# Optimization experiments

Hardware: AMD Instinct MI355X
Metric: run time of the kernel (lower is better)

Reference implementation:

```python
import jax, jax.numpy as jnp
import numpy as np

B, C, T = 128, 8, 128   # batch, channels, time steps
K, S = 20, 128          # known classes, barycenter length


def setup_inputs() -> dict:
    key = jax.random.key(0)
    k1, k2, k3, k4, k5 = jax.random.split(key, 5)
    x = jax.random.normal(k1, (B, C, T), dtype=jnp.float32)
    preds = jax.random.randint(k2, (B,), 0, K).astype(jnp.int32)
    barycenters = jax.random.normal(k3, (K, S, C), dtype=jnp.float32)
    # thresholds centered near realistic scales so both detector branches fire
    top_dist = 7.0 + 0.5 * jax.random.normal(k4, (K,), dtype=jnp.float32)
    bottom_cc = 25.0 + 5.0 * jax.random.normal(k5, (K, C), dtype=jnp.float32)
    return {"x": x, "preds": preds, "barycenters": barycenters,
            "top_dist": top_dist, "bottom_cc": bottom_cc}


def _dtw_dist(cost):
    """Classic DTW DP over a [T, S] sq-euclidean cost matrix; returns accumulated cost."""
    inf = jnp.asarray(jnp.inf, cost.dtype)
    row0 = jnp.cumsum(cost[0])  # first row: only left moves

    def row_step(prev, crow):
        prev_shift = jnp.concatenate([jnp.full((1,), inf, cost.dtype), prev[:-1]])
        def col_step(left, inp):
            c, p, ps = inp
            v = c + jnp.minimum(jnp.minimum(p, ps), left)
            return v, v
        _, row = jax.lax.scan(col_step, inf, (crow, prev, prev_shift))
        return row, None

    last, _ = jax.lax.scan(row_step, row0, cost[1:])
    return last[-1]


def reference(x, preds, barycenters, top_dist, bottom_cc):
    xt = jnp.transpose(x, (0, 2, 1))                    # [B, T, C]
    x2 = jnp.sum(xt * xt, axis=-1)                      # [B, T]
    b2 = jnp.sum(barycenters * barycenters, axis=-1)    # [K, S]
    dots = jnp.einsum('btc,ksc->bkts', xt, barycenters)  # [B, K, T, S]
    cost = jnp.maximum(x2[:, None, :, None] + b2[None, :, None, :] - 2.0 * dots, 0.0)

    Bn, Kn, Tn, Sn = cost.shape
    dists = jax.vmap(_dtw_dist)(cost.reshape(Bn * Kn, Tn, Sn)).reshape(Bn, Kn)
    log_dists = jnp.log(dists)
    dtw_unknown = jnp.all(log_dists > top_dist[None, :], axis=1)   # [B]

    # per-channel full cross-correlation max vs each barycenter
    corr_max = lambda a, v: jnp.max(jnp.correlate(a, v, mode='full'))
    per_ch = jax.vmap(corr_max, in_axes=(1, 1))          # over channels -> [C]
    per_cls = jax.vmap(per_ch, in_axes=(None, 0))        # over classes  -> [K, C]
    per_b = jax.vmap(per_cls, in_axes=(0, None))         # over batch    -> [B, K, C]
    ccs = per_b(xt, barycenters)
    # class 'fails' if any channel cc is not above its bottom threshold
    cc_unknown = jnp.all(jnp.any(ccs <= bottom_cc[None, :, :], axis=2), axis=1)  # [B]

    unknown = cc_unknown | dtw_unknown
    return jnp.where(unknown, Kn, preds)
```

## Files before the change

kernel.cpp:

```cpp
#include <hip/hip_runtime.h>
#include <hip/hip_bf16.h>
#include <math.h>

#define B_ 128
#define C_ 8
#define T_ 128
#define K_ 20
#define S_ 128

#define XROW 388
#define BTROW 132
#define SWZ(j) ((j) ^ ((((j) >> 5) & 7) << 2))
#define XP_GUARD 16
#define BT_BASE (4 * XROW + XP_GUARD)
#define TILEF 1536
#define SMEMF 3680

template <int CTRL, int RMASK>
__device__ __forceinline__ float dppf(float oldv, float v) {
    return __int_as_float(__builtin_amdgcn_update_dpp(
        __float_as_int(oldv), __float_as_int(v), CTRL, RMASK, 0xf, false));
}

__global__ __launch_bounds__(256) void fused_kernel(const float* __restrict__ x,
                                                    const float* __restrict__ bary,
                                                    const float* __restrict__ top_dist,
                                                    const float* __restrict__ bottom_cc,
                                                    int* __restrict__ dtw_gt,
                                                    int* __restrict__ cc_fail2) {
    __shared__ __align__(16) float smem[SMEMF];
    const float INF = __builtin_inff();
    int u = blockIdx.x;
    int tid = threadIdx.x;
    int w = tid >> 6;
    int lane = tid & 63;

    if (u % 5 == 0) {
        int j  = u / 5;
        int p0 = j * 8 + w * 2;
        int b  = p0 / K_;
        int k0 = p0 - b * K_;
        int b_lo = (j * 8) / K_;
        int b_hi = (j * 8 + 7) / K_;
        float* tile0 = smem;
        float* tile1 = smem + TILEF;

        {
            int c  = tid >> 5;
            int t0 = (tid & 31) * 4;
            float4 v0 = *(const float4*)(x + ((size_t)b_lo * C_ + c) * T_ + t0);
            float4 v1 = *(const float4*)(x + ((size_t)b_hi * C_ + c) * T_ + t0);
            tile0[(t0 + 0) * 12 + c] = v0.x;
            tile0[(t0 + 1) * 12 + c] = v0.y;
            tile0[(t0 + 2) * 12 + c] = v0.z;
            tile0[(t0 + 3) * 12 + c] = v0.w;
            tile1[(t0 + 0) * 12 + c] = v1.x;
            tile1[(t0 + 1) * 12 + c] = v1.y;
            tile1[(t0 + 2) * 12 + c] = v1.z;
            tile1[(t0 + 3) * 12 + c] = v1.w;
        }
        __syncthreads();
        {
            float* tt = (tid < T_) ? tile0 : tile1;
            int t = tid & (T_ - 1);
            const float* rp = tt + t * 12;
            float4 xa = *(const float4*)rp;
            float4 xh = *(const float4*)(rp + 4);
            float s = xa.x * xa.x;
            s = fmaf(xa.y, xa.y, s); s = fmaf(xa.z, xa.z, s); s = fmaf(xa.w, xa.w, s);
            s = fmaf(xh.x, xh.x, s); s = fmaf(xh.y, xh.y, s); s = fmaf(xh.z, xh.z, s);
            s = fmaf(xh.w, xh.w, s);
            tt[t * 12 + 8] = s;
        }
        __syncthreads();

        const float* tile = (b == b_lo) ? tile0 : tile1;

        float bvA0[8], bvA1[8], bvB0[8], bvB1[8], B2A0, B2A1, B2B0, B2B1;
        {
            const float4* bpA = (const float4*)(bary + ((size_t)k0 * S_ + 2 * lane) * C_);
            const float4* bpB = (const float4*)(bary + ((size_t)(k0 + 1) * S_ + 2 * lane) * C_);
            float4 qa0 = bpA[0], qa1 = bpA[1], qa2 = bpA[2], qa3 = bpA[3];
            float4 qb0 = bpB[0], qb1 = bpB[1], qb2 = bpB[2], qb3 = bpB[3];
            bvA0[0]=qa0.x; bvA0[1]=qa0.y; bvA0[2]=qa0.z; bvA0[3]=qa0.w;
            bvA0[4]=qa1.x; bvA0[5]=qa1.y; bvA0[6]=qa1.z; bvA0[7]=qa1.w;
            bvA1[0]=qa2.x; bvA1[1]=qa2.y; bvA1[2]=qa2.z; bvA1[3]=qa2.w;
            bvA1[4]=qa3.x; bvA1[5]=qa3.y; bvA1[6]=qa3.z; bvA1[7]=qa3.w;
            bvB0[0]=qb0.x; bvB0[1]=qb0.y; bvB0[2]=qb0.z; bvB0[3]=qb0.w;
            bvB0[4]=qb1.x; bvB0[5]=qb1.y; bvB0[6]=qb1.z; bvB0[7]=qb1.w;
            bvB1[0]=qb2.x; bvB1[1]=qb2.y; bvB1[2]=qb2.z; bvB1[3]=qb2.w;
            bvB1[4]=qb3.x; bvB1[5]=qb3.y; bvB1[6]=qb3.z; bvB1[7]=qb3.w;
            float sA0=0.f, sA1=0.f, sB0=0.f, sB1=0.f;
            #pragma unroll
            for (int ch = 0; ch < 8; ++ch) {
                sA0 = fmaf(bvA0[ch], bvA0[ch], sA0);
                sA1 = fmaf(bvA1[ch], bvA1[ch], sA1);
                sB0 = fmaf(bvB0[ch], bvB0[ch], sB0);
                sB1 = fmaf(bvB1[ch], bvB1[ch], sB1);
            }
            B2A0 = sA0; B2A1 = sA1; B2B0 = sB0; B2B1 = sB1;
            #pragma unroll
            for (int ch = 0; ch < 8; ++ch) {
                bvA0[ch] *= -2.f; bvA1[ch] *= -2.f;
                bvB0[ch] *= -2.f; bvB1[ch] *= -2.f;
            }
        }

        float nA0 = INF, nA1 = INF, nB0 = INF, nB1 = INF;
        float dfix = (lane == 0) ? 0.f : INF;

        __builtin_amdgcn_s_setprio(1);
        float4 xa_n = *(const float4*)tile;
        float4 xh_n = *(const float4*)(tile + 4);
        float x2_n  = tile[8];

        #pragma unroll 2
        for (int t = 0; t < T_; ++t) {
            float4 xa = xa_n, xh = xh_n;
            float X2t = x2_n;
            const float* rpn = tile + ((t + 1) & (T_ - 1)) * 12;
            xa_n = *(const float4*)rpn;
            xh_n = *(const float4*)(rpn + 4);
            x2_n = rpn[8];

            float xv[8];
            xv[0]=xa.x; xv[1]=xa.y; xv[2]=xa.z; xv[3]=xa.w;
            xv[4]=xh.x; xv[5]=xh.y; xv[6]=xh.z; xv[7]=xh.w;
            float aA0 = X2t + B2A0, aA1 = X2t + B2A1;
            float aB0 = X2t + B2B0, aB1 = X2t + B2B1;
            #pragma unroll
            for (int ch = 0; ch < 8; ++ch) {
                aA0 = fmaf(bvA0[ch], xv[ch], aA0);
                aA1 = fmaf(bvA1[ch], xv[ch], aA1);
                aB0 = fmaf(bvB0[ch], xv[ch], aB0);
                aB1 = fmaf(bvB1[ch], xv[ch], aB1);
            }
            aA0 = fmaxf(aA0, 0.f); aA1 = fmaxf(aA1, 0.f);
            aB0 = fmaxf(aB0, 0.f); aB1 = fmaxf(aB1, 0.f);

            float diagA = dppf<0x138, 0xf>(INF, nA1);
            float diagB = dppf<0x138, 0xf>(INF, nB1);
            float mA0 = fminf(fminf(nA0, diagA), dfix);
            float mB0 = fminf(fminf(nB0, diagB), dfix);
            float mA1 = fminf(nA1, nA0);
            float mB1 = fminf(nB1, nB0);
            dfix = INF;
            float CA0 = aA0 + mA0, CA1 = aA1 + mA1;
            float CB0 = aB0 + mB0, CB1 = aB1 + mB1;
            float CA = fminf(CA1, CA0 + aA1);  float AA = aA0 + aA1;
            float CB = fminf(CB1, CB0 + aB1);  float AB = aB0 + aB1;

            float CiA, AiA, CiB, AiB;
            #define SCAN_STEP(CTRL, RMASK)                                          \
                CiA = dppf<CTRL, RMASK>(INF, CA); AiA = dppf<CTRL, RMASK>(0.f, AA); \
                CiB = dppf<CTRL, RMASK>(INF, CB); AiB = dppf<CTRL, RMASK>(0.f, AB); \
                CA = fminf(CA, CiA + AA); AA = AA + AiA;                            \
                CB = fminf(CB, CiB + AB); AB = AB + AiB;
            SCAN_STEP(0x111, 0xf)
            SCAN_STEP(0x112, 0xf)
            SCAN_STEP(0x114, 0xf)
            SCAN_STEP(0x118, 0xf)
            SCAN_STEP(0x142, 0xa)
            SCAN_STEP(0x143, 0xc)
            #undef SCAN_STEP

            float CpA = dppf<0x138, 0xf>(INF, CA);
            float CpB = dppf<0x138, 0xf>(INF, CB);
            nA0 = fminf(CA0, CpA + aA0);  nA1 = CA;
            nB0 = fminf(CB0, CpB + aB0);  nB1 = CB;
        }
        __builtin_amdgcn_s_setprio(0);

        if (lane == 63) {
            dtw_gt[p0]     = (logf(nA1) > top_dist[k0])     ? 1 : 0;
            dtw_gt[p0 + 1] = (logf(nB1) > top_dist[k0 + 1]) ? 1 : 0;
        }
    } else {
        int cb = u - u / 5 - 1;
        int bh = cb / 5;
        int g5 = cb - bh * 5;
        int b  = bh >> 1;
        int h  = bh & 1;
        int kk = g5 * 4 + w;
        int cbase = h * 4;

        float* xp = smem;
        float* bt = smem + BT_BASE + w * (4 * BTROW);

        const float* xsrc = x + ((size_t)b * C_ + cbase) * T_;
        #pragma unroll
        for (int c = 0; c < 4; ++c) {
            for (int jj = tid; jj < XROW; jj += 256) {
                int t = jj - (S_ - 1);
                float v = (t >= 0 && t < T_) ? xsrc[c * T_ + t] : 0.f;
                xp[c * XROW + SWZ(jj)] = v;
            }
        }
        #pragma unroll
        for (int r = 0; r < 2; ++r) {
            int s = r * 64 + lane;
            float4 q = *(const float4*)(bary + ((size_t)kk * S_ + s) * C_ + cbase);
            bt[0 * BTROW + s] = q.x;
            bt[1 * BTROW + s] = q.y;
            bt[2 * BTROW + s] = q.z;
            bt[3 * BTROW + s] = q.w;
        }
        __syncthreads();

        int cl = lane >> 4;
        int gl = lane & 15;
        int lag0 = gl << 4;
        const float* xr = xp + cl * XROW;
        const float* br = bt + cl * BTROW;

        float wdw[20];
        #pragma unroll
        for (int i = 0; i < 5; ++i) {
            float4 v = *(const float4*)&xr[SWZ(lag0 + i * 4)];
            wdw[i * 4 + 0] = v.x; wdw[i * 4 + 1] = v.y;
            wdw[i * 4 + 2] = v.z; wdw[i * 4 + 3] = v.w;
        }
        float acc[16];
        #pragma unroll
        for (int jj = 0; jj < 16; ++jj) acc[jj] = 0.f;

        #pragma unroll 8
        for (int s4 = 0; s4 < S_; s4 += 4) {
            float4 bq = *(const float4*)&br[s4];
            float bvals[4] = {bq.x, bq.y, bq.z, bq.w};
            #pragma unroll
            for (int uu = 0; uu < 4; ++uu) {
                #pragma unroll
                for (int jj = 0; jj < 16; ++jj)
                    acc[jj] = fmaf(wdw[uu + jj], bvals[uu], acc[jj]);
            }
            #pragma unroll
            for (int i = 0; i < 16; ++i) wdw[i] = wdw[i + 4];
            float4 v = *(const float4*)&xr[SWZ(lag0 + s4 + 20)];
            wdw[16] = v.x; wdw[17] = v.y; wdw[18] = v.z; wdw[19] = v.w;
        }

        if (gl == 15) acc[15] = -INF;
        float m = acc[0];
        #pragma unroll
        for (int jj = 1; jj < 16; ++jj) m = fmaxf(m, acc[jj]);
        #pragma unroll
        for (int off = 8; off >= 1; off >>= 1)
            m = fmaxf(m, __shfl_xor(m, off));

        bool fail = false;
        if (gl == 0) fail = (m <= bottom_cc[kk * C_ + cbase + cl]);
        unsigned long long bal = __ballot(fail);
        if (lane == 0) cc_fail2[(b * K_ + kk) * 2 + h] = (bal != 0ULL) ? 1 : 0;
    }
}

__global__ void final_kernel(const int* __restrict__ preds,
                             const int* __restrict__ dtw_gt,
                             const int* __restrict__ cc_fail2,
                             int* __restrict__ out) {
    int b = threadIdx.x;
    if (b < B_) {
        int dtw_all = 1, cc_all = 1;
        #pragma unroll
        for (int k = 0; k < K_; ++k) {
            dtw_all &= dtw_gt[b * K_ + k];
            cc_all &= (cc_fail2[(b * K_ + k) * 2] | cc_fail2[(b * K_ + k) * 2 + 1]);
        }
        out[b] = (dtw_all | cc_all) ? K_ : preds[b];
    }
}

extern "C" void kernel_launch(void* const* d_in, const int* in_sizes, int n_in,
                              void* d_out, int out_size, void* d_ws, size_t ws_size,
                              hipStream_t stream) {
    const float* x         = (const float*)d_in[0];
    const int*   preds     = (const int*)d_in[1];
    const float* bary      = (const float*)d_in[2];
    const float* top_dist  = (const float*)d_in[3];
    const float* bottom_cc = (const float*)d_in[4];
    int* out = (int*)d_out;

    int* dtw_gt   = (int*)d_ws;
    int* cc_fail2 = dtw_gt + B_ * K_;

    fused_kernel<<<1600, 256, 0, stream>>>(x, bary, top_dist, bottom_cc, dtw_gt, cc_fail2);
    final_kernel<<<1, 128, 0, stream>>>(preds, dtw_gt, cc_fail2, out);
}
```

Baseline: 77.78 us.

## Process all channels per cross-correlation block with larger register tiles and rebalanced grid

Each cross-correlation block now handles all 8 channels of a batch row instead of half, and each lane computes 32 lags instead of 16. The lag window becomes a 40-entry rotating register ring, so register shifts are no longer needed. The grid shrinks from 1600 to 960 blocks with a 1:2 ratio of DTW to CC blocks. The DTW loop drops its cost clamp at zero and its unroll, and launch bounds request 4 blocks per CU. Risks include higher register pressure from acc[32] plus wdw[40], larger LDS use, and slightly different results where floating-point rounding would have made a cost negative.

```diff
diff --git a/kernel.cpp b/kernel.cpp
--- a/kernel.cpp
+++ b/kernel.cpp
@@ -8,13 +8,11 @@
 #define K_ 20
 #define S_ 128
 
-#define XROW 388
-#define BTROW 132
 #define SWZ(j) ((j) ^ ((((j) >> 5) & 7) << 2))
-#define XP_GUARD 16
-#define BT_BASE (4 * XROW + XP_GUARD)
+#define XSTR 420
+#define BTSTR 132
 #define TILEF 1536
-#define SMEMF 3680
+#define SMEMF 7584
 
 template <int CTRL, int RMASK>
 __device__ __forceinline__ float dppf(float oldv, float v) {
@@ -22,12 +20,33 @@
         __float_as_int(oldv), __float_as_int(v), CTRL, RMASK, 0xf, false));
 }
 
-__global__ __launch_bounds__(256) void fused_kernel(const float* __restrict__ x,
-                                                    const float* __restrict__ bary,
-                                                    const float* __restrict__ top_dist,
-                                                    const float* __restrict__ bottom_cc,
-                                                    int* __restrict__ dtw_gt,
-                                                    int* __restrict__ cc_fail2) {
+template <int BASE>
+__device__ __forceinline__ void cstep(float (&wdw)[40], float (&acc)[32],
+                                      const float* br, const float* xr,
+                                      int s8, int lag0) {
+    float4 b0 = *(const float4*)&br[s8];
+    float4 b1 = *(const float4*)&br[s8 + 4];
+    float bvv[8] = {b0.x, b0.y, b0.z, b0.w, b1.x, b1.y, b1.z, b1.w};
+    #pragma unroll
+    for (int uu = 0; uu < 8; ++uu) {
+        #pragma unroll
+        for (int jj = 0; jj < 32; ++jj)
+            acc[jj] = fmaf(wdw[(BASE + uu + jj) % 40], bvv[uu], acc[jj]);
+    }
+    float4 p0 = *(const float4*)&xr[SWZ(lag0 + s8 + 40)];
+    float4 p1 = *(const float4*)&xr[SWZ(lag0 + s8 + 44)];
+    wdw[(BASE + 0) % 40] = p0.x; wdw[(BASE + 1) % 40] = p0.y;
+    wdw[(BASE + 2) % 40] = p0.z; wdw[(BASE + 3) % 40] = p0.w;
+    wdw[(BASE + 4) % 40] = p1.x; wdw[(BASE + 5) % 40] = p1.y;
+    wdw[(BASE + 6) % 40] = p1.z; wdw[(BASE + 7) % 40] = p1.w;
+}
+
+__global__ __launch_bounds__(256, 4) void fused_kernel(const float* __restrict__ x,
+                                                       const float* __restrict__ bary,
+                                                       const float* __restrict__ top_dist,
+                                                       const float* __restrict__ bottom_cc,
+                                                       int* __restrict__ dtw_gt,
+                                                       int* __restrict__ cc_fail) {
     __shared__ __align__(16) float smem[SMEMF];
     const float INF = __builtin_inff();
     int u = blockIdx.x;
@@ -35,8 +54,8 @@
     int w = tid >> 6;
     int lane = tid & 63;
 
-    if (u % 5 == 0) {
-        int j  = u / 5;
+    if (u % 3 == 0) {
+        int j  = u / 3;
         int p0 = j * 8 + w * 2;
         int b  = p0 / K_;
         int k0 = p0 - b * K_;
@@ -114,7 +133,7 @@
         float4 xh_n = *(const float4*)(tile + 4);
         float x2_n  = tile[8];
 
-        #pragma unroll 2
+        #pragma unroll 1
         for (int t = 0; t < T_; ++t) {
             float4 xa = xa_n, xh = xh_n;
             float X2t = x2_n;
@@ -135,8 +154,6 @@
                 aB0 = fmaf(bvB0[ch], xv[ch], aB0);
                 aB1 = fmaf(bvB1[ch], xv[ch], aB1);
             }
-            aA0 = fmaxf(aA0, 0.f); aA1 = fmaxf(aA1, 0.f);
-            aB0 = fmaxf(aB0, 0.f); aB1 = fmaxf(aB1, 0.f);
 
             float diagA = dppf<0x138, 0xf>(INF, nA1);
             float diagB = dppf<0x138, 0xf>(INF, nB1);
@@ -176,88 +193,80 @@
             dtw_gt[p0 + 1] = (logf(nB1) > top_dist[k0 + 1]) ? 1 : 0;
         }
     } else {
-        int cb = u - u / 5 - 1;
-        int bh = cb / 5;
-        int g5 = cb - bh * 5;
-        int b  = bh >> 1;
-        int h  = bh & 1;
+        int cb = u - u / 3 - 1;
+        int bb = cb / 5;
+        int g5 = cb - bb * 5;
         int kk = g5 * 4 + w;
-        int cbase = h * 4;
 
         float* xp = smem;
-        float* bt = smem + BT_BASE + w * (4 * BTROW);
-
-        const float* xsrc = x + ((size_t)b * C_ + cbase) * T_;
-        #pragma unroll
-        for (int c = 0; c < 4; ++c) {
-            for (int jj = tid; jj < XROW; jj += 256) {
+        float* bt = smem + 8 * XSTR + w * (8 * BTSTR);
+
+        const float* xsrc = x + (size_t)bb * (C_ * T_);
+        #pragma unroll
+        for (int c = 0; c < 8; ++c) {
+            for (int jj = tid; jj < 392; jj += 256) {
                 int t = jj - (S_ - 1);
                 float v = (t >= 0 && t < T_) ? xsrc[c * T_ + t] : 0.f;
-                xp[c * XROW + SWZ(jj)] = v;
-            }
-        }
-        #pragma unroll
-        for (int r = 0; r < 2; ++r) {
-            int s = r * 64 + lane;
-            float4 q = *(const float4*)(bary + ((size_t)kk * S_ + s) * C_ + cbase);
-            bt[0 * BTROW + s] = q.x;
-            bt[1 * BTROW + s] = q.y;
-            bt[2 * BTROW + s] = q.z;
-            bt[3 * BTROW + s] = q.w;
+                xp[c * XSTR + SWZ(jj)] = v;
+            }
+        }
+        {
+            const float* bp = bary + ((size_t)kk * S_ + 2 * lane) * C_;
+            float4 q0 = *(const float4*)bp,       q1 = *(const float4*)(bp + 4);
+            float4 q2 = *(const float4*)(bp + 8), q3 = *(const float4*)(bp + 12);
+            int s0 = 2 * lane;
+            bt[0*BTSTR+s0]=q0.x; bt[1*BTSTR+s0]=q0.y; bt[2*BTSTR+s0]=q0.z; bt[3*BTSTR+s0]=q0.w;
+            bt[4*BTSTR+s0]=q1.x; bt[5*BTSTR+s0]=q1.y; bt[6*BTSTR+s0]=q1.z; bt[7*BTSTR+s0]=q1.w;
+            bt[0*BTSTR+s0+1]=q2.x; bt[1*BTSTR+s0+1]=q2.y; bt[2*BTSTR+s0+1]=q2.z; bt[3*BTSTR+s0+1]=q2.w;
+            bt[4*BTSTR+s0+1]=q3.x; bt[5*BTSTR+s0+1]=q3.y; bt[6*BTSTR+s0+1]=q3.z; bt[7*BTSTR+s0+1]=q3.w;
         }
         __syncthreads();
 
-        int cl = lane >> 4;
-        int gl = lane & 15;
-        int lag0 = gl << 4;
-        const float* xr = xp + cl * XROW;
-        const float* br = bt + cl * BTROW;
-
-        float wdw[20];
-        #pragma unroll
-        for (int i = 0; i < 5; ++i) {
-            float4 v = *(const float4*)&xr[SWZ(lag0 + i * 4)];
-            wdw[i * 4 + 0] = v.x; wdw[i * 4 + 1] = v.y;
-            wdw[i * 4 + 2] = v.z; wdw[i * 4 + 3] = v.w;
-        }
-        float acc[16];
-        #pragma unroll
-        for (int jj = 0; jj < 16; ++jj) acc[jj] = 0.f;
-
-        #pragma unroll 8
-        for (int s4 = 0; s4 < S_; s4 += 4) {
-            float4 bq = *(const float4*)&br[s4];
-            float bvals[4] = {bq.x, bq.y, bq.z, bq.w};
-            #pragma unroll
-            for (int uu = 0; uu < 4; ++uu) {
-                #pragma unroll
-                for (int jj = 0; jj < 16; ++jj)
-                    acc[jj] = fmaf(wdw[uu + jj], bvals[uu], acc[jj]);
-            }
-            #pragma unroll
-            for (int i = 0; i < 16; ++i) wdw[i] = wdw[i + 4];
-            float4 v = *(const float4*)&xr[SWZ(lag0 + s4 + 20)];
-            wdw[16] = v.x; wdw[17] = v.y; wdw[18] = v.z; wdw[19] = v.w;
-        }
-
-        if (gl == 15) acc[15] = -INF;
+        int g  = lane >> 3;
+        int gl = lane & 7;
+        int lag0 = gl << 5;
+        const float* xr = xp + g * XSTR;
+        const float* br = bt + g * BTSTR;
+
+        float wdw[40];
+        #pragma unroll
+        for (int i = 0; i < 10; ++i) {
+            float4 v = *(const float4*)&xr[SWZ(lag0 + 4 * i)];
+            wdw[4*i+0] = v.x; wdw[4*i+1] = v.y; wdw[4*i+2] = v.z; wdw[4*i+3] = v.w;
+        }
+        float acc[32];
+        #pragma unroll
+        for (int jj = 0; jj < 32; ++jj) acc[jj] = 0.f;
+
+        #pragma unroll 1
+        for (int blk = 0; blk < 3; ++blk) {
+            int s8 = blk * 40;
+            cstep<0 >(wdw, acc, br, xr, s8,      lag0);
+            cstep<8 >(wdw, acc, br, xr, s8 + 8,  lag0);
+            cstep<16>(wdw, acc, br, xr, s8 + 16, lag0);
+            cstep<24>(wdw, acc, br, xr, s8 + 24, lag0);
+            cstep<32>(wdw, acc, br, xr, s8 + 32, lag0);
+        }
+        cstep<0>(wdw, acc, br, xr, 120, lag0);
+
+        if (gl == 7) acc[31] = -INF;
         float m = acc[0];
         #pragma unroll
-        for (int jj = 1; jj < 16; ++jj) m = fmaxf(m, acc[jj]);
-        #pragma unroll
-        for (int off = 8; off >= 1; off >>= 1)
-            m = fmaxf(m, __shfl_xor(m, off));
+        for (int jj = 1; jj < 32; ++jj) m = fmaxf(m, acc[jj]);
+        m = fmaxf(m, __shfl_xor(m, 1));
+        m = fmaxf(m, __shfl_xor(m, 2));
+        m = fmaxf(m, __shfl_xor(m, 4));
 
         bool fail = false;
-        if (gl == 0) fail = (m <= bottom_cc[kk * C_ + cbase + cl]);
+        if (gl == 0) fail = (m <= bottom_cc[kk * C_ + g]);
         unsigned long long bal = __ballot(fail);
-        if (lane == 0) cc_fail2[(b * K_ + kk) * 2 + h] = (bal != 0ULL) ? 1 : 0;
+        if (lane == 0) cc_fail[bb * K_ + kk] = (bal != 0ULL) ? 1 : 0;
     }
 }
 
 __global__ void final_kernel(const int* __restrict__ preds,
                              const int* __restrict__ dtw_gt,
-                             const int* __restrict__ cc_fail2,
+                             const int* __restrict__ cc_fail,
                              int* __restrict__ out) {
     int b = threadIdx.x;
     if (b < B_) {
@@ -265,7 +274,7 @@
         #pragma unroll
         for (int k = 0; k < K_; ++k) {
             dtw_all &= dtw_gt[b * K_ + k];
-            cc_all &= (cc_fail2[(b * K_ + k) * 2] | cc_fail2[(b * K_ + k) * 2 + 1]);
+            cc_all &= cc_fail[b * K_ + k];
         }
         out[b] = (dtw_all | cc_all) ? K_ : preds[b];
     }
@@ -281,9 +290,9 @@
     const float* bottom_cc = (const float*)d_in[4];
     int* out = (int*)d_out;
 
-    int* dtw_gt   = (int*)d_ws;
-    int* cc_fail2 = dtw_gt + B_ * K_;
-
-    fused_kernel<<<1600, 256, 0, stream>>>(x, bary, top_dist, bottom_cc, dtw_gt, cc_fail2);
-    final_kernel<<<1, 128, 0, stream>>>(preds, dtw_gt, cc_fail2, out);
-}
+    int* dtw_gt  = (int*)d_ws;
+    int* cc_fail = dtw_gt + B_ * K_;
+
+    fused_kernel<<<960, 256, 0, stream>>>(x, bary, top_dist, bottom_cc, dtw_gt, cc_fail);
+    final_kernel<<<1, 128, 0, stream>>>(preds, dtw_gt, cc_fail, out);
+}
```

Measured after the change: 89.04 us. 1.14x slower.

## Split fused kernel into DTW and cross-correlation kernels, one DTW pair per wavefront

Applied to the files above, without the earlier changes.

Splits the fused kernel into separate DTW and cross-correlation kernels so each can use its own launch bounds and shared memory size. The DTW kernel now handles one class pair per half-wavefront, with 4 columns per lane and a 5-step DPP scan over 32 lanes instead of 2 columns and 6 steps, which shortens the serial scan per time step. The cc kernel replaces the register shifting of the sliding window with a rotating-index window unrolled in groups of five. The two kernels now run back to back rather than interleaved, which may lose overlap between the DTW and correlation work.

```diff
diff --git a/kernel.cpp b/kernel.cpp
--- a/kernel.cpp
+++ b/kernel.cpp
@@ -8,13 +8,12 @@
 #define K_ 20
 #define S_ 128
 
+#define SWZ(j) ((j) ^ ((((j) >> 5) & 7) << 2))
 #define XROW 388
 #define BTROW 132
-#define SWZ(j) ((j) ^ ((((j) >> 5) & 7) << 2))
 #define XP_GUARD 16
 #define BT_BASE (4 * XROW + XP_GUARD)
 #define TILEF 1536
-#define SMEMF 3680
 
 template <int CTRL, int RMASK>
 __device__ __forceinline__ float dppf(float oldv, float v) {
@@ -22,237 +21,244 @@
         __float_as_int(oldv), __float_as_int(v), CTRL, RMASK, 0xf, false));
 }
 
-__global__ __launch_bounds__(256) void fused_kernel(const float* __restrict__ x,
-                                                    const float* __restrict__ bary,
-                                                    const float* __restrict__ top_dist,
-                                                    const float* __restrict__ bottom_cc,
-                                                    int* __restrict__ dtw_gt,
-                                                    int* __restrict__ cc_fail2) {
-    __shared__ __align__(16) float smem[SMEMF];
+__global__ __launch_bounds__(256, 2) void dtw_kernel(const float* __restrict__ x,
+                                                     const float* __restrict__ bary,
+                                                     const float* __restrict__ top_dist,
+                                                     int* __restrict__ dtw_gt) {
+    __shared__ __align__(16) float smem[2 * TILEF];
     const float INF = __builtin_inff();
     int u = blockIdx.x;
     int tid = threadIdx.x;
     int w = tid >> 6;
     int lane = tid & 63;
 
-    if (u % 5 == 0) {
-        int j  = u / 5;
-        int p0 = j * 8 + w * 2;
-        int b  = p0 / K_;
-        int k0 = p0 - b * K_;
-        int b_lo = (j * 8) / K_;
-        int b_hi = (j * 8 + 7) / K_;
-        float* tile0 = smem;
-        float* tile1 = smem + TILEF;
-
-        {
-            int c  = tid >> 5;
-            int t0 = (tid & 31) * 4;
-            float4 v0 = *(const float4*)(x + ((size_t)b_lo * C_ + c) * T_ + t0);
-            float4 v1 = *(const float4*)(x + ((size_t)b_hi * C_ + c) * T_ + t0);
-            tile0[(t0 + 0) * 12 + c] = v0.x;
-            tile0[(t0 + 1) * 12 + c] = v0.y;
-            tile0[(t0 + 2) * 12 + c] = v0.z;
-            tile0[(t0 + 3) * 12 + c] = v0.w;
-            tile1[(t0 + 0) * 12 + c] = v1.x;
-            tile1[(t0 + 1) * 12 + c] = v1.y;
-            tile1[(t0 + 2) * 12 + c] = v1.z;
-            tile1[(t0 + 3) * 12 + c] = v1.w;
-        }
-        __syncthreads();
-        {
-            float* tt = (tid < T_) ? tile0 : tile1;
-            int t = tid & (T_ - 1);
-            const float* rp = tt + t * 12;
-            float4 xa = *(const float4*)rp;
-            float4 xh = *(const float4*)(rp + 4);
-            float s = xa.x * xa.x;
-            s = fmaf(xa.y, xa.y, s); s = fmaf(xa.z, xa.z, s); s = fmaf(xa.w, xa.w, s);
-            s = fmaf(xh.x, xh.x, s); s = fmaf(xh.y, xh.y, s); s = fmaf(xh.z, xh.z, s);
-            s = fmaf(xh.w, xh.w, s);
-            tt[t * 12 + 8] = s;
-        }
-        __syncthreads();
-
-        const float* tile = (b == b_lo) ? tile0 : tile1;
-
-        float bvA0[8], bvA1[8], bvB0[8], bvB1[8], B2A0, B2A1, B2B0, B2B1;
-        {
-            const float4* bpA = (const float4*)(bary + ((size_t)k0 * S_ + 2 * lane) * C_);
-            const float4* bpB = (const float4*)(bary + ((size_t)(k0 + 1) * S_ + 2 * lane) * C_);
-            float4 qa0 = bpA[0], qa1 = bpA[1], qa2 = bpA[2], qa3 = bpA[3];
-            float4 qb0 = bpB[0], qb1 = bpB[1], qb2 = bpB[2], qb3 = bpB[3];
-            bvA0[0]=qa0.x; bvA0[1]=qa0.y; bvA0[2]=qa0.z; bvA0[3]=qa0.w;
-            bvA0[4]=qa1.x; bvA0[5]=qa1.y; bvA0[6]=qa1.z; bvA0[7]=qa1.w;
-            bvA1[0]=qa2.x; bvA1[1]=qa2.y; bvA1[2]=qa2.z; bvA1[3]=qa2.w;
-            bvA1[4]=qa3.x; bvA1[5]=qa3.y; bvA1[6]=qa3.z; bvA1[7]=qa3.w;
-            bvB0[0]=qb0.x; bvB0[1]=qb0.y; bvB0[2]=qb0.z; bvB0[3]=qb0.w;
-            bvB0[4]=qb1.x; bvB0[5]=qb1.y; bvB0[6]=qb1.z; bvB0[7]=qb1.w;
-            bvB1[0]=qb2.x; bvB1[1]=qb2.y; bvB1[2]=qb2.z; bvB1[3]=qb2.w;
-            bvB1[4]=qb3.x; bvB1[5]=qb3.y; bvB1[6]=qb3.z; bvB1[7]=qb3.w;
-            float sA0=0.f, sA1=0.f, sB0=0.f, sB1=0.f;
+    int wid = u * 4 + w;
+    int p0  = 2 * wid;
+    int b   = p0 / K_;
+    int k0  = p0 - b * K_;
+    int b_lo = (8 * u) / K_;
+    int b_hi = (8 * u + 7) / K_;
+    float* tile0 = smem;
+    float* tile1 = smem + TILEF;
+
+    {
+        int c  = tid >> 5;
+        int t0 = (tid & 31) * 4;
+        float4 v0 = *(const float4*)(x + ((size_t)b_lo * C_ + c) * T_ + t0);
+        float4 v1 = *(const float4*)(x + ((size_t)b_hi * C_ + c) * T_ + t0);
+        tile0[(t0 + 0) * 12 + c] = v0.x;
+        tile0[(t0 + 1) * 12 + c] = v0.y;
+        tile0[(t0 + 2) * 12 + c] = v0.z;
+        tile0[(t0 + 3) * 12 + c] = v0.w;
+        tile1[(t0 + 0) * 12 + c] = v1.x;
+        tile1[(t0 + 1) * 12 + c] = v1.y;
+        tile1[(t0 + 2) * 12 + c] = v1.z;
+        tile1[(t0 + 3) * 12 + c] = v1.w;
+    }
+    __syncthreads();
+    {
+        float* tt = (tid < T_) ? tile0 : tile1;
+        int t = tid & (T_ - 1);
+        const float* rp = tt + t * 12;
+        float4 xa = *(const float4*)rp;
+        float4 xh = *(const float4*)(rp + 4);
+        float s = xa.x * xa.x;
+        s = fmaf(xa.y, xa.y, s); s = fmaf(xa.z, xa.z, s); s = fmaf(xa.w, xa.w, s);
+        s = fmaf(xh.x, xh.x, s); s = fmaf(xh.y, xh.y, s); s = fmaf(xh.z, xh.z, s);
+        s = fmaf(xh.w, xh.w, s);
+        tt[t * 12 + 8] = s;
+    }
+    __syncthreads();
+
+    const float* tile = (b == b_lo) ? tile0 : tile1;
+
+    int g  = lane >> 5;
+    int gl = lane & 31;
+    int kx = k0 + g;
+
+    float bv[4][8], B2s[4];
+    {
+        const float4* bp = (const float4*)(bary + ((size_t)kx * S_ + 4 * gl) * C_);
+        #pragma unroll
+        for (int r = 0; r < 4; ++r) {
+            float4 q0 = bp[2 * r], q1 = bp[2 * r + 1];
+            bv[r][0] = q0.x; bv[r][1] = q0.y; bv[r][2] = q0.z; bv[r][3] = q0.w;
+            bv[r][4] = q1.x; bv[r][5] = q1.y; bv[r][6] = q1.z; bv[r][7] = q1.w;
+            float s = 0.f;
             #pragma unroll
-            for (int ch = 0; ch < 8; ++ch) {
-                sA0 = fmaf(bvA0[ch], bvA0[ch], sA0);
-                sA1 = fmaf(bvA1[ch], bvA1[ch], sA1);
-                sB0 = fmaf(bvB0[ch], bvB0[ch], sB0);
-                sB1 = fmaf(bvB1[ch], bvB1[ch], sB1);
-            }
-            B2A0 = sA0; B2A1 = sA1; B2B0 = sB0; B2B1 = sB1;
+            for (int ch = 0; ch < 8; ++ch) s = fmaf(bv[r][ch], bv[r][ch], s);
+            B2s[r] = s;
             #pragma unroll
-            for (int ch = 0; ch < 8; ++ch) {
-                bvA0[ch] *= -2.f; bvA1[ch] *= -2.f;
-                bvB0[ch] *= -2.f; bvB1[ch] *= -2.f;
-            }
-        }
-
-        float nA0 = INF, nA1 = INF, nB0 = INF, nB1 = INF;
-        float dfix = (lane == 0) ? 0.f : INF;
-
-        __builtin_amdgcn_s_setprio(1);
-        float4 xa_n = *(const float4*)tile;
-        float4 xh_n = *(const float4*)(tile + 4);
-        float x2_n  = tile[8];
-
-        #pragma unroll 2
-        for (int t = 0; t < T_; ++t) {
-            float4 xa = xa_n, xh = xh_n;
-            float X2t = x2_n;
-            const float* rpn = tile + ((t + 1) & (T_ - 1)) * 12;
-            xa_n = *(const float4*)rpn;
-            xh_n = *(const float4*)(rpn + 4);
-            x2_n = rpn[8];
-
-            float xv[8];
-            xv[0]=xa.x; xv[1]=xa.y; xv[2]=xa.z; xv[3]=xa.w;
-            xv[4]=xh.x; xv[5]=xh.y; xv[6]=xh.z; xv[7]=xh.w;
-            float aA0 = X2t + B2A0, aA1 = X2t + B2A1;
-            float aB0 = X2t + B2B0, aB1 = X2t + B2B1;
-            #pragma unroll
-            for (int ch = 0; ch < 8; ++ch) {
-                aA0 = fmaf(bvA0[ch], xv[ch], aA0);
-                aA1 = fmaf(bvA1[ch], xv[ch], aA1);
-                aB0 = fmaf(bvB0[ch], xv[ch], aB0);
-                aB1 = fmaf(bvB1[ch], xv[ch], aB1);
-            }
-            aA0 = fmaxf(aA0, 0.f); aA1 = fmaxf(aA1, 0.f);
-            aB0 = fmaxf(aB0, 0.f); aB1 = fmaxf(aB1, 0.f);
-
-            float diagA = dppf<0x138, 0xf>(INF, nA1);
-            float diagB = dppf<0x138, 0xf>(INF, nB1);
-            float mA0 = fminf(fminf(nA0, diagA), dfix);
-            float mB0 = fminf(fminf(nB0, diagB), dfix);
-            float mA1 = fminf(nA1, nA0);
-            float mB1 = fminf(nB1, nB0);
-            dfix = INF;
-            float CA0 = aA0 + mA0, CA1 = aA1 + mA1;
-            float CB0 = aB0 + mB0, CB1 = aB1 + mB1;
-            float CA = fminf(CA1, CA0 + aA1);  float AA = aA0 + aA1;
-            float CB = fminf(CB1, CB0 + aB1);  float AB = aB0 + aB1;
-
-            float CiA, AiA, CiB, AiB;
-            #define SCAN_STEP(CTRL, RMASK)                                          \
-                CiA = dppf<CTRL, RMASK>(INF, CA); AiA = dppf<CTRL, RMASK>(0.f, AA); \
-                CiB = dppf<CTRL, RMASK>(INF, CB); AiB = dppf<CTRL, RMASK>(0.f, AB); \
-                CA = fminf(CA, CiA + AA); AA = AA + AiA;                            \
-                CB = fminf(CB, CiB + AB); AB = AB + AiB;
-            SCAN_STEP(0x111, 0xf)
-            SCAN_STEP(0x112, 0xf)
-            SCAN_STEP(0x114, 0xf)
-            SCAN_STEP(0x118, 0xf)
-            SCAN_STEP(0x142, 0xa)
-            SCAN_STEP(0x143, 0xc)
-            #undef SCAN_STEP
-
-            float CpA = dppf<0x138, 0xf>(INF, CA);
-            float CpB = dppf<0x138, 0xf>(INF, CB);
-            nA0 = fminf(CA0, CpA + aA0);  nA1 = CA;
-            nB0 = fminf(CB0, CpB + aB0);  nB1 = CB;
-        }
-        __builtin_amdgcn_s_setprio(0);
-
-        if (lane == 63) {
-            dtw_gt[p0]     = (logf(nA1) > top_dist[k0])     ? 1 : 0;
-            dtw_gt[p0 + 1] = (logf(nB1) > top_dist[k0 + 1]) ? 1 : 0;
-        }
-    } else {
-        int cb = u - u / 5 - 1;
-        int bh = cb / 5;
-        int g5 = cb - bh * 5;
-        int b  = bh >> 1;
-        int h  = bh & 1;
-        int kk = g5 * 4 + w;
-        int cbase = h * 4;
-
-        float* xp = smem;
-        float* bt = smem + BT_BASE + w * (4 * BTROW);
-
-        const float* xsrc = x + ((size_t)b * C_ + cbase) * T_;
-        #pragma unroll
-        for (int c = 0; c < 4; ++c) {
-            for (int jj = tid; jj < XROW; jj += 256) {
-                int t = jj - (S_ - 1);
-                float v = (t >= 0 && t < T_) ? xsrc[c * T_ + t] : 0.f;
-                xp[c * XROW + SWZ(jj)] = v;
-            }
-        }
-        #pragma unroll
-        for (int r = 0; r < 2; ++r) {
-            int s = r * 64 + lane;
-            float4 q = *(const float4*)(bary + ((size_t)kk * S_ + s) * C_ + cbase);
-            bt[0 * BTROW + s] = q.x;
-            bt[1 * BTROW + s] = q.y;
-            bt[2 * BTROW + s] = q.z;
-            bt[3 * BTROW + s] = q.w;
-        }
-        __syncthreads();
-
-        int cl = lane >> 4;
-        int gl = lane & 15;
-        int lag0 = gl << 4;
-        const float* xr = xp + cl * XROW;
-        const float* br = bt + cl * BTROW;
-
-        float wdw[20];
-        #pragma unroll
-        for (int i = 0; i < 5; ++i) {
-            float4 v = *(const float4*)&xr[SWZ(lag0 + i * 4)];
-            wdw[i * 4 + 0] = v.x; wdw[i * 4 + 1] = v.y;
-            wdw[i * 4 + 2] = v.z; wdw[i * 4 + 3] = v.w;
-        }
-        float acc[16];
-        #pragma unroll
-        for (int jj = 0; jj < 16; ++jj) acc[jj] = 0.f;
-
-        #pragma unroll 8
-        for (int s4 = 0; s4 < S_; s4 += 4) {
-            float4 bq = *(const float4*)&br[s4];
-            float bvals[4] = {bq.x, bq.y, bq.z, bq.w};
-            #pragma unroll
-            for (int uu = 0; uu < 4; ++uu) {
-                #pragma unroll
-                for (int jj = 0; jj < 16; ++jj)
-                    acc[jj] = fmaf(wdw[uu + jj], bvals[uu], acc[jj]);
-            }
-            #pragma unroll
-            for (int i = 0; i < 16; ++i) wdw[i] = wdw[i + 4];
-            float4 v = *(const float4*)&xr[SWZ(lag0 + s4 + 20)];
-            wdw[16] = v.x; wdw[17] = v.y; wdw[18] = v.z; wdw[19] = v.w;
-        }
-
-        if (gl == 15) acc[15] = -INF;
-        float m = acc[0];
-        #pragma unroll
-        for (int jj = 1; jj < 16; ++jj) m = fmaxf(m, acc[jj]);
-        #pragma unroll
-        for (int off = 8; off >= 1; off >>= 1)
-            m = fmaxf(m, __shfl_xor(m, off));
-
-        bool fail = false;
-        if (gl == 0) fail = (m <= bottom_cc[kk * C_ + cbase + cl]);
-        unsigned long long bal = __ballot(fail);
-        if (lane == 0) cc_fail2[(b * K_ + kk) * 2 + h] = (bal != 0ULL) ? 1 : 0;
-    }
+            for (int ch = 0; ch < 8; ++ch) bv[r][ch] *= -2.f;
+        }
+    }
+
+    bool isg0 = (gl == 0);
+    float n0 = INF, n1 = INF, n2 = INF, n3 = INF;
+    float dfix = isg0 ? 0.f : INF;
+
+    float4 xa_n = *(const float4*)tile;
+    float4 xh_n = *(const float4*)(tile + 4);
+    float x2_n  = tile[8];
+
+    #pragma unroll 2
+    for (int t = 0; t < T_; ++t) {
+        float4 xa = xa_n, xh = xh_n;
+        float X2t = x2_n;
+        const float* rpn = tile + ((t + 1) & (T_ - 1)) * 12;
+        xa_n = *(const float4*)rpn;
+        xh_n = *(const float4*)(rpn + 4);
+        x2_n = rpn[8];
+
+        float xv[8];
+        xv[0]=xa.x; xv[1]=xa.y; xv[2]=xa.z; xv[3]=xa.w;
+        xv[4]=xh.x; xv[5]=xh.y; xv[6]=xh.z; xv[7]=xh.w;
+        float a0 = X2t + B2s[0], a1 = X2t + B2s[1];
+        float a2 = X2t + B2s[2], a3 = X2t + B2s[3];
+        #pragma unroll
+        for (int ch = 0; ch < 8; ++ch) {
+            a0 = fmaf(bv[0][ch], xv[ch], a0);
+            a1 = fmaf(bv[1][ch], xv[ch], a1);
+            a2 = fmaf(bv[2][ch], xv[ch], a2);
+            a3 = fmaf(bv[3][ch], xv[ch], a3);
+        }
+
+        float dl = dppf<0x138, 0xf>(INF, n3);
+        float diag = isg0 ? INF : dl;
+        float m0 = fminf(fminf(n0, diag), dfix);
+        float m1 = fminf(n1, n0);
+        float m2 = fminf(n2, n1);
+        float m3 = fminf(n3, n2);
+        dfix = INF;
+        float C0 = a0 + m0, C1 = a1 + m1, C2 = a2 + m2, C3 = a3 + m3;
+        float A01  = a0 + a1;
+        float C01  = fminf(C1, C0 + a1);
+        float A012 = A01 + a2;
+        float C012 = fminf(C2, C01 + a2);
+        float A    = A012 + a3;
+        float C    = fminf(C3, C012 + a3);
+
+        float Ci, Ai;
+        #define SCAN_STEP(CTRL, RMASK)                                         \
+            Ci = dppf<CTRL, RMASK>(INF, C); Ai = dppf<CTRL, RMASK>(0.f, A);    \
+            C = fminf(C, Ci + A); A = A + Ai;
+        SCAN_STEP(0x111, 0xf)
+        SCAN_STEP(0x112, 0xf)
+        SCAN_STEP(0x114, 0xf)
+        SCAN_STEP(0x118, 0xf)
+        SCAN_STEP(0x142, 0xa)
+        #undef SCAN_STEP
+
+        float Cpw = dppf<0x138, 0xf>(INF, C);
+        float Cp  = isg0 ? INF : Cpw;
+        n0 = fminf(C0,   Cp + a0);
+        n1 = fminf(C01,  Cp + A01);
+        n2 = fminf(C012, Cp + A012);
+        n3 = C;
+    }
+
+    if (gl == 31)
+        dtw_gt[p0 + g] = (logf(n3) > top_dist[kx]) ? 1 : 0;
+}
+
+template <int BASE>
+__device__ __forceinline__ void cstep4(float (&wdw)[20], float (&acc)[16],
+                                       const float* br, const float* xr,
+                                       int s4, int lag0) {
+    float4 bq = *(const float4*)&br[s4];
+    float bvv[4] = {bq.x, bq.y, bq.z, bq.w};
+    #pragma unroll
+    for (int uu = 0; uu < 4; ++uu) {
+        #pragma unroll
+        for (int jj = 0; jj < 16; ++jj)
+            acc[jj] = fmaf(wdw[(BASE + uu + jj) % 20], bvv[uu], acc[jj]);
+    }
+    float4 p = *(const float4*)&xr[SWZ(lag0 + s4 + 20)];
+    wdw[(BASE + 0) % 20] = p.x; wdw[(BASE + 1) % 20] = p.y;
+    wdw[(BASE + 2) % 20] = p.z; wdw[(BASE + 3) % 20] = p.w;
+}
+
+__global__ __launch_bounds__(256, 4) void cc_kernel(const float* __restrict__ x,
+                                                    const float* __restrict__ bary,
+                                                    const float* __restrict__ bottom_cc,
+                                                    int* __restrict__ cc_fail2) {
+    __shared__ __align__(16) float smem[BT_BASE + 4 * 8 * BTROW];
+    const float INF = __builtin_inff();
+    int cb = blockIdx.x;
+    int tid = threadIdx.x;
+    int w = tid >> 6;
+    int lane = tid & 63;
+
+    int bh = cb / 5;
+    int g5 = cb - bh * 5;
+    int b  = bh >> 1;
+    int h  = bh & 1;
+    int kk = g5 * 4 + w;
+    int cbase = h * 4;
+
+    float* xp = smem;
+    float* bt = smem + BT_BASE + w * (4 * BTROW);
+
+    const float* xsrc = x + ((size_t)b * C_ + cbase) * T_;
+    #pragma unroll
+    for (int c = 0; c < 4; ++c) {
+        for (int jj = tid; jj < XROW; jj += 256) {
+            int t = jj - (S_ - 1);
+            float v = (t >= 0 && t < T_) ? xsrc[c * T_ + t] : 0.f;
+            xp[c * XROW + SWZ(jj)] = v;
+        }
+    }
+    #pragma unroll
+    for (int r = 0; r < 2; ++r) {
+        int s = r * 64 + lane;
+        float4 q = *(const float4*)(bary + ((size_t)kk * S_ + s) * C_ + cbase);
+        bt[0 * BTROW + s] = q.x;
+        bt[1 * BTROW + s] = q.y;
+        bt[2 * BTROW + s] = q.z;
+        bt[3 * BTROW + s] = q.w;
+    }
+    __syncthreads();
+
+    int cl = lane >> 4;
+    int gl = lane & 15;
+    int lag0 = gl << 4;
+    const float* xr = xp + cl * XROW;
+    const float* br = bt + cl * BTROW;
+
+    float wdw[20];
+    #pragma unroll
+    for (int i = 0; i < 5; ++i) {
+        float4 v = *(const float4*)&xr[SWZ(lag0 + 4 * i)];
+        wdw[4*i+0] = v.x; wdw[4*i+1] = v.y; wdw[4*i+2] = v.z; wdw[4*i+3] = v.w;
+    }
+    float acc[16];
+    #pragma unroll
+    for (int jj = 0; jj < 16; ++jj) acc[jj] = 0.f;
+
+    #pragma unroll 1
+    for (int it = 0; it < 6; ++it) {
+        int s4 = it * 20;
+        cstep4<0 >(wdw, acc, br, xr, s4,      lag0);
+        cstep4<4 >(wdw, acc, br, xr, s4 + 4,  lag0);
+        cstep4<8 >(wdw, acc, br, xr, s4 + 8,  lag0);
+        cstep4<12>(wdw, acc, br, xr, s4 + 12, lag0);
+        cstep4<16>(wdw, acc, br, xr, s4 + 16, lag0);
+    }
+    cstep4<0>(wdw, acc, br, xr, 120, lag0);
+    cstep4<4>(wdw, acc, br, xr, 124, lag0);
+
+    if (gl == 15) acc[15] = -INF;
+    float m = acc[0];
+    #pragma unroll
+    for (int jj = 1; jj < 16; ++jj) m = fmaxf(m, acc[jj]);
+    #pragma unroll
+    for (int off = 8; off >= 1; off >>= 1)
+        m = fmaxf(m, __shfl_xor(m, off));
+
+    bool fail = false;
+    if (gl == 0) fail = (m <= bottom_cc[kk * C_ + cbase + cl]);
+    unsigned long long bal = __ballot(fail);
+    if (lane == 0) cc_fail2[(b * K_ + kk) * 2 + h] = (bal != 0ULL) ? 1 : 0;
 }
 
 __global__ void final_kernel(const int* __restrict__ preds,
@@ -284,6 +290,7 @@
     int* dtw_gt   = (int*)d_ws;
     int* cc_fail2 = dtw_gt + B_ * K_;
 
-    fused_kernel<<<1600, 256, 0, stream>>>(x, bary, top_dist, bottom_cc, dtw_gt, cc_fail2);
+    dtw_kernel<<<320, 256, 0, stream>>>(x, bary, top_dist, dtw_gt);
+    cc_kernel<<<1280, 256, 0, stream>>>(x, bary, bottom_cc, cc_fail2);
     final_kernel<<<1, 128, 0, stream>>>(preds, dtw_gt, cc_fail2, out);
 }
```

After: 65.78 us. 15.4% less time.
